# Kernel tuning notes

Hardware: AMD Instinct MI355X
Metric: run time of the kernel (lower is better)

The kernel has to match this reference:

```python
import jax, jax.numpy as jnp
import numpy as np

B, ORDER, S, D, H = 64, 2, 256, 256, 8
HD = D // H  # head_dim = 32


def setup_inputs() -> dict:
    key = jax.random.key(0)
    ks = jax.random.split(key, 6)
    stdv = 1.0 / np.sqrt(HD)
    return {
        "x": jax.random.normal(ks[0], (B, ORDER, S, D), jnp.float32),
        "A": jax.random.randint(ks[1], (B, ORDER, S, S), 0, 5, jnp.int32),
        # params stacked as [order, conv(1|2), ...]
        "Wp": jax.random.normal(ks[2], (ORDER, 2, D, D), jnp.float32) * stdv,
        "bp": jnp.zeros((ORDER, 2, D), jnp.float32),
        "att_src": jax.random.normal(ks[3], (ORDER, 2, H, HD), jnp.float32) * stdv,
        "att_dst": jax.random.normal(ks[4], (ORDER, 2, H, HD), jnp.float32) * stdv,
        "gbias": jnp.zeros((ORDER, 2, D), jnp.float32),
        "prelu_a": 0.25 * jnp.ones((D,), jnp.float32),
    }


def _gat(x, edge, W, b, a_src, a_dst, gb):
    """Dense additive GAT over a [B,S,S] boolean adjacency. Eval mode (dropout inert)."""
    Bt, St, Dt = x.shape
    x = x @ W + b                                   # project (bias=True)
    xh = x.reshape(Bt, St, H, HD)
    a_s = jnp.einsum('bshd,hd->bsh', xh, a_src)     # per-source score
    a_d = jnp.einsum('bthd,hd->bth', xh, a_dst)     # per-dest score
    alpha = a_s[:, :, None, :] + a_d[:, None, :, :]  # [B, S_src, S_dst, H]
    alpha = jnp.where(edge[..., None], alpha, 0.0)   # masked_fill((A != 1), 0)
    alpha = jnp.where(alpha >= 0, alpha, 0.2 * alpha)  # leaky_relu(0.2)
    alpha = jax.nn.softmax(alpha, axis=1)            # stable softmax over source axis
    out = jnp.einsum('bsth,bshd->bthd', alpha, xh).reshape(Bt, St, Dt)
    return out + x + gb                              # add_self_loops + bias


def reference(x, A, Wp, bp, att_src, att_dst, gbias, prelu_a):
    # A1 = (A==2)+(A==4); A2 = (A==3)+(A==4); edge iff value == 1
    A1 = (A == 2) | (A == 4)
    A2 = (A == 3) | (A == 4)
    hs = []
    for i in range(ORDER):  # order is a small structural constant (=2)
        h1 = _gat(x[:, i], A1[:, i], Wp[i, 0], bp[i, 0], att_src[i, 0], att_dst[i, 0], gbias[i, 0])
        h2 = _gat(x[:, i], A2[:, i], Wp[i, 1], bp[i, 1], att_src[i, 1], att_dst[i, 1], gbias[i, 1])
        hs.append(h1 + h2)
    h = jnp.stack(hs, axis=1)                       # [B, order, S, D]
    out = h + h.mean(axis=1, keepdims=True)
    out = jnp.where(out >= 0, out, prelu_a * out)   # PReLU(dim)
    return out
```

## Files before the change

kernel.cpp:

```cpp
#include <hip/hip_runtime.h>
#include <hip/hip_bf16.h>
#include <math.h>

typedef __bf16 bf16;
typedef __bf16 bf16x4 __attribute__((ext_vector_type(4)));
typedef __bf16 bf16x8 __attribute__((ext_vector_type(8)));
typedef float f32x4 __attribute__((ext_vector_type(4)));
typedef unsigned int u32;

#define LOG2E 1.44269504f

__device__ inline float fast_exp2(float x) {
#if __has_builtin(__builtin_amdgcn_exp2f)
    return __builtin_amdgcn_exp2f(x);
#else
    return exp2f(x);
#endif
}

#define GL2LDS(gp, lp) __builtin_amdgcn_global_load_lds( \
    (const __attribute__((address_space(1))) u32*)(gp),  \
    (__attribute__((address_space(3))) u32*)(lp), 16, 0, 0)


__global__ void prep_k(const float* __restrict__ x, const float* __restrict__ Wp,
                       const int* __restrict__ A, bf16* __restrict__ xb,
                       bf16* __restrict__ Wt, unsigned* __restrict__ m1,
                       unsigned* __restrict__ m2) {
    int bid = blockIdx.x;
    int tid = threadIdx.x;
    if (bid < 4096) {
        int gid = bid * 256 + tid;
        const f32x4* xp = (const f32x4*)x + (size_t)gid * 2;
        f32x4 a = xp[0], b4 = xp[1];
        bf16x8 o;
#pragma unroll
        for (int c = 0; c < 4; ++c) { o[c] = (bf16)a[c]; o[c + 4] = (bf16)b4[c]; }
        ((bf16x8*)xb)[gid] = o;
    } else if (bid < 5120) {
        int gid = (bid - 4096) * 256 + tid;
        int k = gid & 255;
        int n = (gid >> 8) & 255;
        int ij = gid >> 16;
        Wt[gid] = (bf16)Wp[(ij * 256 + k) * 256 + n];
    } else {
        int pb = bid - 5120;
        int sh = pb & 1;
        int ijb = pb >> 1;
        const int* Ab = A + ((size_t)ijb << 16);
        unsigned w1 = 0, w2 = 0;
#pragma unroll 8
        for (int sl = 0; sl < 128; ++sl) {
            int s = sh * 128 + sl;
            int av = Ab[s * 256 + tid];
            unsigned f1 = (av == 2 || av == 4) ? 1u : 0u;
            unsigned f2 = (av == 3 || av == 4) ? 1u : 0u;
            w1 |= f1 << (s & 31);
            w2 |= f2 << (s & 31);
            if ((s & 31) == 31) {
                int kc = s >> 5;
                m1[(ijb * 8 + kc) * 256 + tid] = w1;
                m2[(ijb * 8 + kc) * 256 + tid] = w2;
                w1 = 0; w2 = 0;
            }
        }
    }
}

__launch_bounds__(256)
__global__ void proj_gemm(const bf16* __restrict__ xb, const bf16* __restrict__ Wt,
                          const float* __restrict__ bp, const float* __restrict__ att_src,
                          const float* __restrict__ att_dst, bf16* __restrict__ Vt,
                          float* __restrict__ asb, float* __restrict__ adb) {
    __shared__ char smem[35840 + 1024];
    bf16* As = (bf16*)smem;
    bf16* Bs = (bf16*)(smem + 8192);
    bf16* TL = (bf16*)smem;
    float* attL = (float*)(smem + 35840);

    int tid = threadIdx.x;
    int mt = blockIdx.x, nt = blockIdx.y, i = blockIdx.z;
    int n0 = nt * 128;
    int j = n0 >> 8, d0 = n0 & 255;
    int ij = i * 2 + j;
    int m0 = mt * 128;
    int b = m0 >> 8, shalf = (m0 >> 7) & 1;

    {
        int which = tid >> 7, rest = tid & 127;
        const float* ap = which ? att_dst : att_src;
        attL[tid] = ap[(ij * 8 + (d0 >> 5) + (rest >> 5)) * 32 + (rest & 31)];
    }

    int c0 = tid, c1 = tid + 256;
    int r0 = c0 >> 2, k80 = (c0 & 3) * 8;
    int r1 = c1 >> 2, k81 = (c1 & 3) * 8;
    const bf16* ga0 = xb + (((size_t)((b * 2 + i) * 256 + shalf * 128 + r0)) << 8) + k80;
    const bf16* ga1 = xb + (((size_t)((b * 2 + i) * 256 + shalf * 128 + r1)) << 8) + k81;
    const bf16* gb0 = Wt + (((size_t)(ij * 256 + d0 + r0)) << 8) + k80;
    const bf16* gb1 = Wt + (((size_t)(ij * 256 + d0 + r1)) << 8) + k81;
    bf16* la0 = As + c0 * 8;
    bf16* la1 = As + c1 * 8;
    bf16* lb0 = Bs + c0 * 8;
    bf16* lb1 = Bs + c1 * 8;

    int wave = tid >> 6, lane = tid & 63;
    int wd = (wave & 1) * 64, ws = (wave >> 1) * 64;
    int lrow = lane & 15, quad = lane >> 4;

    f32x4 acc[4][4];
#pragma unroll
    for (int a = 0; a < 4; ++a)
#pragma unroll
        for (int c = 0; c < 4; ++c) acc[a][c] = (f32x4){0.f, 0.f, 0.f, 0.f};

    for (int kc = 0; kc < 8; ++kc) {
        int k0 = kc * 32;
        GL2LDS(ga0 + k0, la0);
        GL2LDS(ga1 + k0, la1);
        GL2LDS(gb0 + k0, lb0);
        GL2LDS(gb1 + k0, lb1);
        __syncthreads();
        bf16x8 wf[4], xf[4];
#pragma unroll
        for (int dj = 0; dj < 4; ++dj)
            wf[dj] = *(const bf16x8*)&Bs[(wd + dj * 16 + lrow) * 32 + quad * 8];
#pragma unroll
        for (int sj = 0; sj < 4; ++sj)
            xf[sj] = *(const bf16x8*)&As[(ws + sj * 16 + lrow) * 32 + quad * 8];
#pragma unroll
        for (int dj = 0; dj < 4; ++dj)
#pragma unroll
            for (int sj = 0; sj < 4; ++sj)
                acc[dj][sj] = __builtin_amdgcn_mfma_f32_16x16x32_bf16(wf[dj], xf[sj], acc[dj][sj], 0, 0, 0);
        __syncthreads();
    }

#pragma unroll
    for (int dj = 0; dj < 4; ++dj) {
#pragma unroll
        for (int r = 0; r < 4; ++r) {
            int dl = wd + dj * 16 + quad * 4 + r;
            float bias = bp[ij * 256 + d0 + dl];
#pragma unroll
            for (int sj = 0; sj < 4; ++sj)
                TL[dl * 140 + ws + sj * 16 + lrow] = (bf16)(acc[dj][sj][r] + bias);
        }
    }
    __syncthreads();

    {
        int dl = tid >> 1, sh64 = (tid & 1) * 64;
        const bf16* src = TL + dl * 140 + sh64;
        bf16* dst = Vt + (((size_t)(ij * 64 + b)) << 16) + (size_t)(d0 + dl) * 256
                    + shalf * 128 + sh64;
#pragma unroll
        for (int q = 0; q < 16; ++q)
            *(bf16x4*)(dst + q * 4) = *(const bf16x4*)(src + q * 4);
    }

    {
        int s = tid & 127, which = tid >> 7;
        const float* av = attL + which * 128;
        float* outp = which ? adb : asb;
#pragma unroll
        for (int hl = 0; hl < 4; ++hl) {
            float accs = 0.f;
#pragma unroll
            for (int d = 0; d < 32; ++d)
                accs += (float)TL[(hl * 32 + d) * 140 + s] * av[hl * 32 + d];
            int hg = (d0 >> 5) + hl;
            outp[((ij * 64 + b) * 8 + hg) * 256 + shalf * 128 + s] = accs * LOG2E;
        }
    }
}

__launch_bounds__(256, 3)
__global__ void attn_k(const bf16* __restrict__ Vt, const unsigned* __restrict__ m1,
                       const unsigned* __restrict__ m2, const float* __restrict__ asb,
                       const float* __restrict__ adb, const float* __restrict__ gbias,
                       float* __restrict__ out) {
    int bid = blockIdx.x;
    int tt = bid & 3, hg = (bid >> 2) & 1, i = (bid >> 3) & 1, b = bid >> 4;
    int t0 = tt * 64;
    int tid = threadIdx.x, wave = tid >> 6, lane = tid & 63;
    int lrow = lane & 15, quad = lane >> 4;
    int h = hg * 4 + wave;

    __shared__ float    as_l[2][4][256];
    __shared__ unsigned ml[2][8][64];
    __shared__ float    l_lds[2][4][64];

#pragma unroll
    for (int p = 0; p < 8; ++p) {
        int c = p >> 2, w = p & 3;
        as_l[c][w][tid] = asb[(((i * 2 + c) * 64 + b) * 8 + hg * 4 + w) * 256 + tid];
    }
    {
        const unsigned* mp0 = m1 + ((b * 2 + i) * 8) * 256 + t0;
        const unsigned* mp1 = m2 + ((b * 2 + i) * 8) * 256 + t0;
#pragma unroll
        for (int p = 0; p < 4; ++p) {
            int idx = p * 256 + tid;
            int c = idx >> 9, kc = (idx >> 6) & 7, tl = idx & 63;
            ml[c][kc][tl] = (c == 0 ? mp0 : mp1)[kc * 256 + tl];
        }
    }
    float ad_r[2][4];
#pragma unroll
    for (int c = 0; c < 2; ++c)
#pragma unroll
        for (int mi = 0; mi < 4; ++mi)
            ad_r[c][mi] = adb[(((i * 2 + c) * 64 + b) * 8 + h) * 256 + t0 + mi * 16 + lrow];
    __syncthreads();

    const bf16* vt0 = Vt + (((size_t)(((i * 2 + 0) * 64 + b) * 8 + h)) << 13);
    const bf16* vt1 = Vt + (((size_t)(((i * 2 + 1) * 64 + b) * 8 + h)) << 13);

    f32x4 acc[2][4][2];
#pragma unroll
    for (int c = 0; c < 2; ++c)
#pragma unroll
        for (int mi = 0; mi < 4; ++mi)
#pragma unroll
            for (int ni = 0; ni < 2; ++ni) acc[c][mi][ni] = (f32x4){0.f, 0.f, 0.f, 0.f};
    float lsum[2][4] = {{0.f, 0.f, 0.f, 0.f}, {0.f, 0.f, 0.f, 0.f}};

    for (int kc = 0; kc < 8; ++kc) {
        int s0 = kc * 32;
        bf16x8 bfr[2][2];
#pragma unroll
        for (int ni = 0; ni < 2; ++ni) {
            bfr[0][ni] = *(const bf16x8*)(vt0 + (size_t)(ni * 16 + lrow) * 256 + s0 + quad * 8);
            bfr[1][ni] = *(const bf16x8*)(vt1 + (size_t)(ni * 16 + lrow) * 256 + s0 + quad * 8);
        }
#pragma unroll
        for (int c = 0; c < 2; ++c) {
            float asv[8];
#pragma unroll
            for (int j = 0; j < 8; ++j) asv[j] = as_l[c][wave][s0 + quad * 8 + j];
#pragma unroll
            for (int mi = 0; mi < 4; ++mi) {
                unsigned wb = ml[c][kc][mi * 16 + lrow] >> (quad * 8);
                float ad = ad_r[c][mi];
                bf16x8 af;
#pragma unroll
                for (int j = 0; j < 8; ++j) {
                    float u = asv[j] + ad;
                    u = fmaxf(u, 0.2f * u);
                    u = ((wb >> j) & 1u) ? u : 0.f;
                    float e = fast_exp2(u);
                    lsum[c][mi] += e;
                    af[j] = (bf16)e;
                }
                acc[c][mi][0] = __builtin_amdgcn_mfma_f32_16x16x32_bf16(af, bfr[c][0], acc[c][mi][0], 0, 0, 0);
                acc[c][mi][1] = __builtin_amdgcn_mfma_f32_16x16x32_bf16(af, bfr[c][1], acc[c][mi][1], 0, 0, 0);
            }
        }
    }

#pragma unroll
    for (int c = 0; c < 2; ++c)
#pragma unroll
        for (int mi = 0; mi < 4; ++mi) {
            float l = lsum[c][mi];
            l += __shfl_xor(l, 16, 64);
            l += __shfl_xor(l, 32, 64);
            if (lane < 16) l_lds[c][wave][mi * 16 + lane] = l;
        }
    __syncthreads();

#pragma unroll
    for (int ni = 0; ni < 2; ++ni) {
        int dcol = h * 32 + ni * 16 + lrow;
        float gb = gbias[(i * 2 + 0) * 256 + dcol] + gbias[(i * 2 + 1) * 256 + dcol];
        const bf16* r0 = vt0 + (size_t)(ni * 16 + lrow) * 256 + t0;
        const bf16* r1 = vt1 + (size_t)(ni * 16 + lrow) * 256 + t0;
#pragma unroll
        for (int mi = 0; mi < 4; ++mi) {
            bf16x4 rv0 = *(const bf16x4*)(r0 + mi * 16 + quad * 4);
            bf16x4 rv1 = *(const bf16x4*)(r1 + mi * 16 + quad * 4);
#pragma unroll
            for (int r = 0; r < 4; ++r) {
                int tl = mi * 16 + quad * 4 + r;
                int t = t0 + tl;
                float inv1 = __builtin_amdgcn_rcpf(l_lds[0][wave][tl]);
                float inv2 = __builtin_amdgcn_rcpf(l_lds[1][wave][tl]);
                float res = (float)rv0[r] + (float)rv1[r];
                float v = acc[0][mi][ni][r] * inv1 + acc[1][mi][ni][r] * inv2 + res + gb;
                out[(((size_t)((b * 2 + i) * 256 + t)) << 8) + dcol] = v;
            }
        }
    }
}

__global__ void final_k(float* __restrict__ out, const float* __restrict__ prelu_a) {
    int gid = blockIdx.x * 256 + threadIdx.x;
    int d4 = gid & 63;
    int s  = (gid >> 6) & 255;
    int b  = gid >> 14;
    f32x4* o = (f32x4*)out;
    size_t i0 = (((size_t)(b * 2 + 0) * 256 + s) << 6) + d4;
    size_t i1 = (((size_t)(b * 2 + 1) * 256 + s) << 6) + d4;
    f32x4 h0 = o[i0], h1 = o[i1];
    f32x4 pa = *(const f32x4*)(prelu_a + d4 * 4);
    f32x4 v0, v1;
#pragma unroll
    for (int c = 0; c < 4; ++c) {
        float mn = 0.5f * (h0[c] + h1[c]);
        float a0 = h0[c] + mn;
        float a1 = h1[c] + mn;
        v0[c] = a0 >= 0.f ? a0 : pa[c] * a0;
        v1[c] = a1 >= 0.f ? a1 : pa[c] * a1;
    }
    o[i0] = v0;
    o[i1] = v1;
}

extern "C" void kernel_launch(void* const* d_in, const int* in_sizes, int n_in,
                              void* d_out, int out_size, void* d_ws, size_t ws_size,
                              hipStream_t stream) {
    const float* x       = (const float*)d_in[0];
    const int*   A       = (const int*)d_in[1];
    const float* Wp      = (const float*)d_in[2];
    const float* bp      = (const float*)d_in[3];
    const float* att_src = (const float*)d_in[4];
    const float* att_dst = (const float*)d_in[5];
    const float* gbias   = (const float*)d_in[6];
    const float* prelu_a = (const float*)d_in[7];
    float* out = (float*)d_out;

    char* ws = (char*)d_ws;
    bf16*     Wt  = (bf16*)ws;
    unsigned* m1  = (unsigned*)(ws + 524288);
    unsigned* m2  = (unsigned*)(ws + 1572864);
    float*    asb = (float*)(ws + 2621440);
    float*    adb = (float*)(ws + 4718592);
    bf16*     xb  = (bf16*)(ws + 6815744);
    bf16*     Vt  = (bf16*)(ws + 23592960);

    prep_k<<<5376, 256, 0, stream>>>(x, Wp, A, xb, Wt, m1, m2);
    dim3 gproj(128, 4, 2);
    proj_gemm<<<gproj, 256, 0, stream>>>(xb, Wt, bp, att_src, att_dst, Vt, asb, adb);
    attn_k<<<1024, 256, 0, stream>>>(Vt, m1, m2, asb, adb, gbias, out);
    final_k<<<4096, 256, 0, stream>>>(out, prelu_a);
}
```

Baseline: 210.4 us.

## Fuse order-mean and PReLU epilogue into attention kernel, both orders per block

Result: no change. 212.0 us (+0.8%).

```diff
diff --git a/kernel.cpp b/kernel.cpp
--- a/kernel.cpp
+++ b/kernel.cpp
@@ -175,146 +175,153 @@
     }
 }
 
-__launch_bounds__(256, 3)
+__launch_bounds__(256, 2)
 __global__ void attn_k(const bf16* __restrict__ Vt, const unsigned* __restrict__ m1,
                        const unsigned* __restrict__ m2, const float* __restrict__ asb,
                        const float* __restrict__ adb, const float* __restrict__ gbias,
-                       float* __restrict__ out) {
+                       const float* __restrict__ prelu_a, float* __restrict__ out) {
     int bid = blockIdx.x;
-    int tt = bid & 3, hg = (bid >> 2) & 1, i = (bid >> 3) & 1, b = bid >> 4;
+    int tt = bid & 3, hg = (bid >> 2) & 1, b = bid >> 3;
     int t0 = tt * 64;
     int tid = threadIdx.x, wave = tid >> 6, lane = tid & 63;
     int lrow = lane & 15, quad = lane >> 4;
     int h = hg * 4 + wave;
 
-    __shared__ float    as_l[2][4][256];
-    __shared__ unsigned ml[2][8][64];
-    __shared__ float    l_lds[2][4][64];
-
+    __shared__ float    as_l[2][2][4][256];
+    __shared__ unsigned ml[2][2][8][64];
+    __shared__ float    l_lds[2][2][4][64];
+
+#pragma unroll
+    for (int p = 0; p < 16; ++p) {
+        int idx = p * 256 + tid;
+        int i = idx >> 11, c = (idx >> 10) & 1, w = (idx >> 8) & 3, s = idx & 255;
+        as_l[i][c][w][s] = asb[(((i * 2 + c) * 64 + b) * 8 + hg * 4 + w) * 256 + s];
+    }
 #pragma unroll
     for (int p = 0; p < 8; ++p) {
-        int c = p >> 2, w = p & 3;
-        as_l[c][w][tid] = asb[(((i * 2 + c) * 64 + b) * 8 + hg * 4 + w) * 256 + tid];
-    }
-    {
-        const unsigned* mp0 = m1 + ((b * 2 + i) * 8) * 256 + t0;
-        const unsigned* mp1 = m2 + ((b * 2 + i) * 8) * 256 + t0;
-#pragma unroll
-        for (int p = 0; p < 4; ++p) {
-            int idx = p * 256 + tid;
-            int c = idx >> 9, kc = (idx >> 6) & 7, tl = idx & 63;
-            ml[c][kc][tl] = (c == 0 ? mp0 : mp1)[kc * 256 + tl];
-        }
-    }
-    float ad_r[2][4];
-#pragma unroll
-    for (int c = 0; c < 2; ++c)
-#pragma unroll
-        for (int mi = 0; mi < 4; ++mi)
-            ad_r[c][mi] = adb[(((i * 2 + c) * 64 + b) * 8 + h) * 256 + t0 + mi * 16 + lrow];
+        int idx = p * 256 + tid;
+        int i = idx >> 10, c = (idx >> 9) & 1, kc = (idx >> 6) & 7, tl = idx & 63;
+        ml[i][c][kc][tl] = (c ? m2 : m1)[((b * 2 + i) * 8 + kc) * 256 + t0 + tl];
+    }
+    float ad_r[2][2][4];
+#pragma unroll
+    for (int i = 0; i < 2; ++i)
+#pragma unroll
+        for (int c = 0; c < 2; ++c)
+#pragma unroll
+            for (int mi = 0; mi < 4; ++mi)
+                ad_r[i][c][mi] = adb[(((i * 2 + c) * 64 + b) * 8 + h) * 256 + t0 + mi * 16 + lrow];
     __syncthreads();
 
-    const bf16* vt0 = Vt + (((size_t)(((i * 2 + 0) * 64 + b) * 8 + h)) << 13);
-    const bf16* vt1 = Vt + (((size_t)(((i * 2 + 1) * 64 + b) * 8 + h)) << 13);
-
-    f32x4 acc[2][4][2];
-#pragma unroll
-    for (int c = 0; c < 2; ++c)
-#pragma unroll
-        for (int mi = 0; mi < 4; ++mi)
-#pragma unroll
-            for (int ni = 0; ni < 2; ++ni) acc[c][mi][ni] = (f32x4){0.f, 0.f, 0.f, 0.f};
-    float lsum[2][4] = {{0.f, 0.f, 0.f, 0.f}, {0.f, 0.f, 0.f, 0.f}};
+    const bf16* vtp[2][2];
+#pragma unroll
+    for (int i = 0; i < 2; ++i)
+#pragma unroll
+        for (int c = 0; c < 2; ++c)
+            vtp[i][c] = Vt + (((size_t)(((i * 2 + c) * 64 + b) * 8 + h)) << 13);
+
+    f32x4 acc[2][2][4][2];
+#pragma unroll
+    for (int i = 0; i < 2; ++i)
+#pragma unroll
+        for (int c = 0; c < 2; ++c)
+#pragma unroll
+            for (int mi = 0; mi < 4; ++mi)
+#pragma unroll
+                for (int ni = 0; ni < 2; ++ni) acc[i][c][mi][ni] = (f32x4){0.f, 0.f, 0.f, 0.f};
+    float lsum[2][2][4];
+#pragma unroll
+    for (int i = 0; i < 2; ++i)
+#pragma unroll
+        for (int c = 0; c < 2; ++c)
+#pragma unroll
+            for (int mi = 0; mi < 4; ++mi) lsum[i][c][mi] = 0.f;
 
     for (int kc = 0; kc < 8; ++kc) {
         int s0 = kc * 32;
-        bf16x8 bfr[2][2];
-#pragma unroll
-        for (int ni = 0; ni < 2; ++ni) {
-            bfr[0][ni] = *(const bf16x8*)(vt0 + (size_t)(ni * 16 + lrow) * 256 + s0 + quad * 8);
-            bfr[1][ni] = *(const bf16x8*)(vt1 + (size_t)(ni * 16 + lrow) * 256 + s0 + quad * 8);
-        }
-#pragma unroll
-        for (int c = 0; c < 2; ++c) {
-            float asv[8];
-#pragma unroll
-            for (int j = 0; j < 8; ++j) asv[j] = as_l[c][wave][s0 + quad * 8 + j];
+        bf16x8 bfr[2][2][2];
+#pragma unroll
+        for (int i = 0; i < 2; ++i)
+#pragma unroll
+            for (int c = 0; c < 2; ++c)
+#pragma unroll
+                for (int ni = 0; ni < 2; ++ni)
+                    bfr[i][c][ni] = *(const bf16x8*)(vtp[i][c] + (size_t)(ni * 16 + lrow) * 256 + s0 + quad * 8);
+#pragma unroll
+        for (int i = 0; i < 2; ++i) {
+#pragma unroll
+            for (int c = 0; c < 2; ++c) {
+                f32x4 asv0 = *(const f32x4*)&as_l[i][c][wave][s0 + quad * 8];
+                f32x4 asv1 = *(const f32x4*)&as_l[i][c][wave][s0 + quad * 8 + 4];
+#pragma unroll
+                for (int mi = 0; mi < 4; ++mi) {
+                    unsigned wb = ml[i][c][kc][mi * 16 + lrow] >> (quad * 8);
+                    float ad = ad_r[i][c][mi];
+                    bf16x8 af;
+#pragma unroll
+                    for (int j = 0; j < 8; ++j) {
+                        float u = (j < 4 ? asv0[j] : asv1[j - 4]) + ad;
+                        u = fmaxf(u, 0.2f * u);
+                        u = ((wb >> j) & 1u) ? u : 0.f;
+                        float e = fast_exp2(u);
+                        lsum[i][c][mi] += e;
+                        af[j] = (bf16)e;
+                    }
+                    acc[i][c][mi][0] = __builtin_amdgcn_mfma_f32_16x16x32_bf16(af, bfr[i][c][0], acc[i][c][mi][0], 0, 0, 0);
+                    acc[i][c][mi][1] = __builtin_amdgcn_mfma_f32_16x16x32_bf16(af, bfr[i][c][1], acc[i][c][mi][1], 0, 0, 0);
+                }
+            }
+        }
+    }
+
+#pragma unroll
+    for (int i = 0; i < 2; ++i)
+#pragma unroll
+        for (int c = 0; c < 2; ++c)
 #pragma unroll
             for (int mi = 0; mi < 4; ++mi) {
-                unsigned wb = ml[c][kc][mi * 16 + lrow] >> (quad * 8);
-                float ad = ad_r[c][mi];
-                bf16x8 af;
-#pragma unroll
-                for (int j = 0; j < 8; ++j) {
-                    float u = asv[j] + ad;
-                    u = fmaxf(u, 0.2f * u);
-                    u = ((wb >> j) & 1u) ? u : 0.f;
-                    float e = fast_exp2(u);
-                    lsum[c][mi] += e;
-                    af[j] = (bf16)e;
-                }
-                acc[c][mi][0] = __builtin_amdgcn_mfma_f32_16x16x32_bf16(af, bfr[c][0], acc[c][mi][0], 0, 0, 0);
-                acc[c][mi][1] = __builtin_amdgcn_mfma_f32_16x16x32_bf16(af, bfr[c][1], acc[c][mi][1], 0, 0, 0);
+                float l = lsum[i][c][mi];
+                l += __shfl_xor(l, 16, 64);
+                l += __shfl_xor(l, 32, 64);
+                if (lane < 16) l_lds[i][c][wave][mi * 16 + lane] = l;
             }
-        }
-    }
-
-#pragma unroll
-    for (int c = 0; c < 2; ++c)
-#pragma unroll
-        for (int mi = 0; mi < 4; ++mi) {
-            float l = lsum[c][mi];
-            l += __shfl_xor(l, 16, 64);
-            l += __shfl_xor(l, 32, 64);
-            if (lane < 16) l_lds[c][wave][mi * 16 + lane] = l;
-        }
     __syncthreads();
 
 #pragma unroll
     for (int ni = 0; ni < 2; ++ni) {
         int dcol = h * 32 + ni * 16 + lrow;
-        float gb = gbias[(i * 2 + 0) * 256 + dcol] + gbias[(i * 2 + 1) * 256 + dcol];
-        const bf16* r0 = vt0 + (size_t)(ni * 16 + lrow) * 256 + t0;
-        const bf16* r1 = vt1 + (size_t)(ni * 16 + lrow) * 256 + t0;
+        float gb0 = gbias[0 * 256 + dcol] + gbias[1 * 256 + dcol];
+        float gb1 = gbias[2 * 256 + dcol] + gbias[3 * 256 + dcol];
+        float pa = prelu_a[dcol];
+        const bf16* r00 = vtp[0][0] + (size_t)(ni * 16 + lrow) * 256 + t0;
+        const bf16* r01 = vtp[0][1] + (size_t)(ni * 16 + lrow) * 256 + t0;
+        const bf16* r10 = vtp[1][0] + (size_t)(ni * 16 + lrow) * 256 + t0;
+        const bf16* r11 = vtp[1][1] + (size_t)(ni * 16 + lrow) * 256 + t0;
 #pragma unroll
         for (int mi = 0; mi < 4; ++mi) {
-            bf16x4 rv0 = *(const bf16x4*)(r0 + mi * 16 + quad * 4);
-            bf16x4 rv1 = *(const bf16x4*)(r1 + mi * 16 + quad * 4);
+            bf16x4 rv00 = *(const bf16x4*)(r00 + mi * 16 + quad * 4);
+            bf16x4 rv01 = *(const bf16x4*)(r01 + mi * 16 + quad * 4);
+            bf16x4 rv10 = *(const bf16x4*)(r10 + mi * 16 + quad * 4);
+            bf16x4 rv11 = *(const bf16x4*)(r11 + mi * 16 + quad * 4);
 #pragma unroll
             for (int r = 0; r < 4; ++r) {
                 int tl = mi * 16 + quad * 4 + r;
                 int t = t0 + tl;
-                float inv1 = __builtin_amdgcn_rcpf(l_lds[0][wave][tl]);
-                float inv2 = __builtin_amdgcn_rcpf(l_lds[1][wave][tl]);
-                float res = (float)rv0[r] + (float)rv1[r];
-                float v = acc[0][mi][ni][r] * inv1 + acc[1][mi][ni][r] * inv2 + res + gb;
-                out[(((size_t)((b * 2 + i) * 256 + t)) << 8) + dcol] = v;
+                float v0 = acc[0][0][mi][ni][r] * __builtin_amdgcn_rcpf(l_lds[0][0][wave][tl])
+                         + acc[0][1][mi][ni][r] * __builtin_amdgcn_rcpf(l_lds[0][1][wave][tl])
+                         + (float)rv00[r] + (float)rv01[r] + gb0;
+                float v1 = acc[1][0][mi][ni][r] * __builtin_amdgcn_rcpf(l_lds[1][0][wave][tl])
+                         + acc[1][1][mi][ni][r] * __builtin_amdgcn_rcpf(l_lds[1][1][wave][tl])
+                         + (float)rv10[r] + (float)rv11[r] + gb1;
+                float mn = 0.5f * (v0 + v1);
+                float a0 = v0 + mn, a1 = v1 + mn;
+                a0 = a0 >= 0.f ? a0 : pa * a0;
+                a1 = a1 >= 0.f ? a1 : pa * a1;
+                out[(((size_t)((b * 2 + 0) * 256 + t)) << 8) + dcol] = a0;
+                out[(((size_t)((b * 2 + 1) * 256 + t)) << 8) + dcol] = a1;
             }
         }
     }
-}
-
-__global__ void final_k(float* __restrict__ out, const float* __restrict__ prelu_a) {
-    int gid = blockIdx.x * 256 + threadIdx.x;
-    int d4 = gid & 63;
-    int s  = (gid >> 6) & 255;
-    int b  = gid >> 14;
-    f32x4* o = (f32x4*)out;
-    size_t i0 = (((size_t)(b * 2 + 0) * 256 + s) << 6) + d4;
-    size_t i1 = (((size_t)(b * 2 + 1) * 256 + s) << 6) + d4;
-    f32x4 h0 = o[i0], h1 = o[i1];
-    f32x4 pa = *(const f32x4*)(prelu_a + d4 * 4);
-    f32x4 v0, v1;
-#pragma unroll
-    for (int c = 0; c < 4; ++c) {
-        float mn = 0.5f * (h0[c] + h1[c]);
-        float a0 = h0[c] + mn;
-        float a1 = h1[c] + mn;
-        v0[c] = a0 >= 0.f ? a0 : pa[c] * a0;
-        v1[c] = a1 >= 0.f ? a1 : pa[c] * a1;
-    }
-    o[i0] = v0;
-    o[i1] = v1;
 }
 
 extern "C" void kernel_launch(void* const* d_in, const int* in_sizes, int n_in,
@@ -342,6 +349,5 @@
     prep_k<<<5376, 256, 0, stream>>>(x, Wp, A, xb, Wt, m1, m2);
     dim3 gproj(128, 4, 2);
     proj_gemm<<<gproj, 256, 0, stream>>>(xb, Wt, bp, att_src, att_dst, Vt, asb, adb);
-    attn_k<<<1024, 256, 0, stream>>>(Vt, m1, m2, asb, adb, gbias, out);
-    final_k<<<4096, 256, 0, stream>>>(out, prelu_a);
-}
+    attn_k<<<512, 256, 0, stream>>>(Vt, m1, m2, asb, adb, gbias, prelu_a, out);
+}
```
